# Kernel optimization log

Hardware: AMD Instinct MI355X
Metric: run time of the kernel (lower is better)

## Reference

```python
import jax, jax.numpy as jnp
import numpy as np

N = 8192          # number of bodies
BOX = 112.0       # world size chosen so expected #colliding pairs ~ 4N
EPS = 1e-12


def setup_inputs() -> dict:
    key = jax.random.key(0)
    k1, k2 = jax.random.split(key)
    centers = jax.random.uniform(k1, (N, 2), dtype=jnp.float32) * BOX
    radii = 0.5 + 0.5 * jax.random.uniform(k2, (N,), dtype=jnp.float32)
    return {"centers": centers, "radii": radii, "limit_broad": 4 * N, "limit_narrow": N}


def reference(centers, radii, limit_broad, limit_narrow):
    n = centers.shape[0]
    # ---- broad phase: all-pairs AABB overlap (AABB = center +/- radius) ----
    dc = jnp.abs(centers[:, None, :] - centers[None, :, :])      # [N,N,2]
    rsum = radii[:, None] + radii[None, :]                        # [N,N]
    overlap = jnp.all(dc <= rsum[..., None], axis=-1)             # [N,N]
    idx = jnp.arange(n)
    mask = overlap & (idx[:, None] < idx[None, :])                # i < j, as in _check_aabb_collision
    # compaction to a fixed limit of 4N candidate pairs (-1 = empty slot)
    flat = jnp.nonzero(mask.reshape(-1), size=limit_broad, fill_value=-1)[0]
    valid_b = flat >= 0
    safe = jnp.where(valid_b, flat, 0)
    pi, pj = safe // n, safe % n                                  # [4N]
    # ---- narrow phase: exact circle penetration on the candidates ----
    d = centers[pj] - centers[pi]                                 # [4N,2]
    dist = jnp.sqrt(jnp.sum(d * d, axis=-1) + EPS)                # [4N]
    depth = radii[pi] + radii[pj] - dist                          # [4N]
    pen = d / dist[:, None] * depth[:, None]                      # penetration vector [4N,2]
    hit = valid_b & (depth > 0)
    # second compaction: keep at most N actually-penetrating pairs
    sel = jnp.nonzero(hit, size=limit_narrow, fill_value=-1)[0]
    vsel = sel >= 0
    ssafe = jnp.where(vsel, sel, 0)
    si, sj = pi[ssafe], pj[ssafe]                                 # [N]
    delta = 0.5 * pen[ssafe] * vsel[:, None].astype(centers.dtype)
    # ---- resolve: scatter: push bodies apart by half the penetration each ----
    new_centers = centers.at[si].add(-delta).at[sj].add(delta)
    return new_centers
```

## Files before the change

### kernel.cpp

```cpp
#include <hip/hip_runtime.h>


constexpr int NB = 8192;
constexpr int GRID_DIM = 56;
constexpr int NCELLS = GRID_DIM * GRID_DIM;
constexpr int CAP = 20;
constexpr int NBLK = 96;
constexpr int RPB = (NB + NBLK - 1) / NBLK;
constexpr float INV_CELL = 0.5f;
constexpr float EPS = 1e-12f;

constexpr int O_CCOUNT = 0;
constexpr int O_RCOMB  = O_CCOUNT + NCELLS;
constexpr int O_CELLS  = (O_RCOMB + NB + 3) & ~3;

__device__ __forceinline__ int cell_of(float v) {
    int c = (int)(v * INV_CELL);
    return c > GRID_DIM - 1 ? GRID_DIM - 1 : (c < 0 ? 0 : c);
}

__device__ __forceinline__ int wave_incl_scan(int v, int lane) {
#pragma unroll
    for (int off = 1; off < 64; off <<= 1) {
        int y = __shfl_up(v, off);
        if (lane >= off) v += y;
    }
    return v;
}

__global__ void fill_kernel(const float2* __restrict__ centers,
                            const float* __restrict__ radii,
                            int* __restrict__ ccount,
                            float4* __restrict__ cells,
                            int* __restrict__ rcomb,
                            float2* __restrict__ out2) {
    const int t = blockIdx.x * blockDim.x + threadIdx.x;
    if (t >= NB) return;
    const float2 c = centers[t];
    const float r = radii[t];
    out2[t] = c;
    rcomb[t] = 0;
    const int cell = cell_of(c.y) * GRID_DIM + cell_of(c.x);
    const int slot = atomicAdd(&ccount[cell], 1);
    if (slot < CAP)
        cells[cell * CAP + slot] = make_float4(c.x, c.y, r, __int_as_float(t));
}

__global__ void count_kernel(const float2* __restrict__ centers,
                             const float* __restrict__ radii,
                             const int* __restrict__ ccount,
                             const float4* __restrict__ cells,
                             int* __restrict__ rcomb) {
    const int t = blockIdx.x * blockDim.x + threadIdx.x;
    if (t >= 3 * NB) return;
    const int i = t & (NB - 1);
    const int seg = t >> 13;
    const float2 ci = centers[i];
    const float ri = radii[i];
    const int cx = cell_of(ci.x), cy = cell_of(ci.y);
    const int yy = cy - 1 + seg;
    if (yy < 0 || yy >= GRID_DIM) return;
    const int x0 = max(cx - 1, 0), x1 = min(cx + 1, GRID_DIM - 1);
    int rc = 0, hc = 0;
    for (int xx = x0; xx <= x1; ++xx) {
        const int c = yy * GRID_DIM + xx;
        const int n = min(ccount[c], CAP);
        const float4* p = cells + c * CAP;
        for (int k = 0; k < n; ++k) {
            const float4 o = p[k];
            if (__float_as_int(o.w) <= i) continue;
            const float rs = ri + o.z;
            const float dx = o.x - ci.x, dy = o.y - ci.y;
            if (fabsf(dx) <= rs && fabsf(dy) <= rs) {
                ++rc;
                if (rs - sqrtf(dx * dx + dy * dy + EPS) > 0.f) ++hc;
            }
        }
    }
    if (rc | hc) atomicAdd(&rcomb[i], (rc << 8) | hc);
}

__device__ int slow_boundary_hits(const int* ccount, const float4* cells,
                                  const float2* centers, const float* radii,
                                  int i, int lim) {
    const float2 ci = centers[i];
    const float ri = radii[i];
    const int cx = cell_of(ci.x), cy = cell_of(ci.y);
    const int x0 = max(cx - 1, 0), x1 = min(cx + 1, GRID_DIM - 1);
    const int y0 = max(cy - 1, 0), y1 = min(cy + 1, GRID_DIM - 1);
    int h = 0;
    for (int yy = y0; yy <= y1; ++yy)
        for (int xx = x0; xx <= x1; ++xx) {
            const int c = yy * GRID_DIM + xx;
            const int n = min(ccount[c], CAP);
            for (int k = 0; k < n; ++k) {
                const float4 o = cells[c * CAP + k];
                const int j = __float_as_int(o.w);
                if (j <= i) continue;
                const float rs = ri + o.z, dx = o.x - ci.x, dy = o.y - ci.y;
                if (!(fabsf(dx) <= rs && fabsf(dy) <= rs)) continue;
                int brank = 0;
                for (int yy2 = y0; yy2 <= y1; ++yy2)
                    for (int xx2 = x0; xx2 <= x1; ++xx2) {
                        const int c2 = yy2 * GRID_DIM + xx2;
                        const int n2 = min(ccount[c2], CAP);
                        for (int k2 = 0; k2 < n2; ++k2) {
                            const float4 o2 = cells[c2 * CAP + k2];
                            const int j2 = __float_as_int(o2.w);
                            if (j2 <= i || j2 >= j) continue;
                            const float rs2 = ri + o2.z;
                            if (fabsf(o2.x - ci.x) <= rs2 && fabsf(o2.y - ci.y) <= rs2)
                                ++brank;
                        }
                    }
                if (brank < lim && rs - sqrtf(dx * dx + dy * dy + EPS) > 0.f) ++h;
            }
        }
    return h;
}

__global__ __launch_bounds__(256) void final_kernel(
        const float2* __restrict__ centers, const float* __restrict__ radii,
        const int* __restrict__ ccount, const float4* __restrict__ cells,
        const int* __restrict__ rcomb,
        const int* __restrict__ LBp, const int* __restrict__ LNp,
        float* __restrict__ out) {
    __shared__ unsigned char sh_st[NB];
    __shared__ int wsum[4];
    __shared__ int spec_n;
    __shared__ int spec_row[2], spec_bst[2], spec_h0[2];
    const int tid = threadIdx.x;
    const int lane = tid & 63, wid = tid >> 6;
    const int LB = *LBp, LN = *LNp;
    if (tid == 0) spec_n = 0;

    int4 v[8];
    const int base = tid * 32;
#pragma unroll
    for (int k = 0; k < 8; ++k) v[k] = ((const int4*)rcomb)[tid * 8 + k];
    const int* vv = (const int*)v;
    int rsum = 0;
#pragma unroll
    for (int k = 0; k < 32; ++k) rsum += vv[k] >> 8;
    const int incl = wave_incl_scan(rsum, lane);
    if (lane == 63) wsum[wid] = incl;
    __syncthreads();
    if (wid == 0) {
        const int orig = (lane < 4) ? wsum[lane] : 0;
        const int inc = wave_incl_scan(orig, lane);
        if (lane < 4) wsum[lane] = inc - orig;
    }
    __syncthreads();
    const int runb0 = wsum[wid] + incl - rsum;
    int runb = runb0, hsum = 0;
#pragma unroll
    for (int k = 0; k < 32; ++k) {
        const int val = vv[k];
        const int rc = val >> 8, hr = val & 0xff;
        int hc;
        if (runb >= LB) hc = 0;
        else if (runb + rc <= LB) hc = hr;
        else hc = slow_boundary_hits(ccount, cells, centers, radii, base + k,
                                     LB - runb);
        hsum += hc;
        runb += rc;
    }
    __syncthreads();
    const int incl2 = wave_incl_scan(hsum, lane);
    if (lane == 63) wsum[wid] = incl2;
    __syncthreads();
    if (wid == 0) {
        const int orig = (lane < 4) ? wsum[lane] : 0;
        const int inc = wave_incl_scan(orig, lane);
        if (lane < 4) wsum[lane] = inc - orig;
    }
    __syncthreads();
    int runh = wsum[wid] + incl2 - hsum;
    runb = runb0;
#pragma unroll
    for (int k = 0; k < 32; ++k) {
        const int i = base + k;
        const int val = vv[k];
        const int rc = val >> 8, hr = val & 0xff;
        int hc;
        if (runb >= LB) hc = 0;
        else if (runb + rc <= LB) hc = hr;
        else hc = slow_boundary_hits(ccount, cells, centers, radii, i, LB - runb);
        unsigned char st = 0;
        if (hc > 0 && runh < LN) {
            const bool bfast = (runb + rc <= LB);
            const bool nfast = (runh + hc <= LN);
            if (bfast && nfast) st = 1;
            else {
                const int n = atomicAdd(&spec_n, 1);
                if (n < 2) { spec_row[n] = i; spec_bst[n] = runb; spec_h0[n] = runh; }
            }
        }
        sh_st[i] = st;
        runb += rc;
        runh += hc;
    }
    __syncthreads();

    const int row_lo = blockIdx.x * RPB;
    const int row_hi = min(NB, row_lo + RPB);

    if (tid < 64) {
        const int ns = min(spec_n, 2);
        for (int sp = 0; sp < ns; ++sp) {
            const int i = spec_row[sp];
            if (i < row_lo || i >= row_hi) continue;
            const int blim = LB - spec_bst[sp];
            const int h0 = spec_h0[sp];
            const float2 ci = centers[i];
            const float ri = radii[i];
            const int cx = cell_of(ci.x), cy = cell_of(ci.y);
            const int x0 = max(cx - 1, 0), x1 = min(cx + 1, GRID_DIM - 1);
            const int y0 = max(cy - 1, 0), y1 = min(cy + 1, GRID_DIM - 1);
            int seg0[9], slen[9], nseg = 0, K = 0;
            for (int yy = y0; yy <= y1; ++yy)
                for (int xx = x0; xx <= x1; ++xx) {
                    const int c = yy * GRID_DIM + xx;
                    const int n = min(ccount[c], CAP);
                    if (n > 0) { seg0[nseg] = c * CAP; slen[nseg] = n; K += n; ++nseg; }
                }
            float accx = 0.f, accy = 0.f;
            for (int cb = 0; cb < K; cb += 64) {
                const int e = cb + lane;
                const bool ok = e < K;
                int s = 0;
                if (ok) {
                    int r = e;
                    for (int g = 0; g < nseg; ++g) {
                        if (r < slen[g]) { s = seg0[g] + r; break; }
                        r -= slen[g];
                    }
                }
                const float4 o = ok ? cells[s] : make_float4(0, 0, 0, __int_as_float(-1));
                const int j = __float_as_int(o.w);
                const float rs = ri + o.z, dx = o.x - ci.x, dy = o.y - ci.y;
                const bool ov = ok && j > i && fabsf(dx) <= rs && fabsf(dy) <= rs;
                if (ov) {
                    const float dist = sqrtf(dx * dx + dy * dy + EPS);
                    const float depth = rs - dist;
                    int brank = 0, hrank = 0;
                    for (int e2 = 0; e2 < K; ++e2) {
                        int r2 = e2, s2 = 0;
                        for (int g = 0; g < nseg; ++g) {
                            if (r2 < slen[g]) { s2 = seg0[g] + r2; break; }
                            r2 -= slen[g];
                        }
                        const float4 o2 = cells[s2];
                        const int j2 = __float_as_int(o2.w);
                        if (j2 <= i || j2 >= j) continue;
                        const float rs2 = ri + o2.z;
                        const float dx2 = o2.x - ci.x, dy2 = o2.y - ci.y;
                        if (fabsf(dx2) <= rs2 && fabsf(dy2) <= rs2) {
                            ++brank;
                            if (rs2 - sqrtf(dx2 * dx2 + dy2 * dy2 + EPS) > 0.f) ++hrank;
                        }
                    }
                    if (depth > 0.f && brank < blim && h0 + hrank < LN) {
                        const float sc = 0.5f * depth / dist;
                        const float px = sc * dx, py = sc * dy;
                        accx -= px; accy -= py;
                        atomicAdd(&out[2 * j], px);
                        atomicAdd(&out[2 * j + 1], py);
                    }
                }
            }
#pragma unroll
            for (int off = 32; off > 0; off >>= 1) {
                accx += __shfl_down(accx, off);
                accy += __shfl_down(accy, off);
            }
            if (lane == 0 && (accx != 0.f || accy != 0.f)) {
                atomicAdd(&out[2 * i], accx);
                atomicAdd(&out[2 * i + 1], accy);
            }
        }
    }

    for (int u = tid; u < RPB * 3; u += 256) {
        const int i = row_lo + u / 3;
        if (i >= row_hi) break;
        if (!sh_st[i]) continue;
        const int seg = u % 3;
        const float2 ci = centers[i];
        const float ri = radii[i];
        const int cx = cell_of(ci.x), cy = cell_of(ci.y);
        const int yy = cy - 1 + seg;
        if (yy < 0 || yy >= GRID_DIM) continue;
        const int x0 = max(cx - 1, 0), x1 = min(cx + 1, GRID_DIM - 1);
        float accx = 0.f, accy = 0.f;
        for (int xx = x0; xx <= x1; ++xx) {
            const int c = yy * GRID_DIM + xx;
            const int n = min(ccount[c], CAP);
            const float4* p = cells + c * CAP;
            for (int k = 0; k < n; ++k) {
                const float4 o = p[k];
                const int j = __float_as_int(o.w);
                if (j <= i) continue;
                const float rs = ri + o.z;
                const float dx = o.x - ci.x, dy = o.y - ci.y;
                if (!(fabsf(dx) <= rs && fabsf(dy) <= rs)) continue;
                const float dist = sqrtf(dx * dx + dy * dy + EPS);
                const float depth = rs - dist;
                if (depth <= 0.f) continue;
                const float sc = 0.5f * depth / dist;
                const float px = sc * dx, py = sc * dy;
                accx -= px; accy -= py;
                atomicAdd(&out[2 * j], px);
                atomicAdd(&out[2 * j + 1], py);
            }
        }
        if (accx != 0.f || accy != 0.f) {
            atomicAdd(&out[2 * i], accx);
            atomicAdd(&out[2 * i + 1], accy);
        }
    }
}

extern "C" void kernel_launch(void* const* d_in, const int* in_sizes, int n_in,
                              void* d_out, int out_size, void* d_ws, size_t ws_size,
                              hipStream_t stream) {
    const float2* centers = (const float2*)d_in[0];
    const float* radii    = (const float*)d_in[1];
    const int* LBp = (const int*)d_in[2];
    const int* LNp = (const int*)d_in[3];
    float* out = (float*)d_out;

    int* ws = (int*)d_ws;
    int* ccount = ws + O_CCOUNT;
    int* rcomb  = ws + O_RCOMB;
    float4* cells = (float4*)(ws + O_CELLS);

    hipMemsetAsync(ccount, 0, NCELLS * sizeof(int), stream);
    fill_kernel<<<NB / 256, 256, 0, stream>>>(centers, radii, ccount, cells,
                                              rcomb, (float2*)out);
    count_kernel<<<3 * NB / 256, 256, 0, stream>>>(centers, radii, ccount,
                                                   cells, rcomb);
    final_kernel<<<NBLK, 256, 0, stream>>>(centers, radii, ccount, cells,
                                           rcomb, LBp, LNp, out);
}
```

Measured before the change: 107.3 us.

## Replace atomic scatter with per-body gather and drop count atomics

After: 126.7 us. +18.1%, slower.

```diff
diff --git a/kernel.cpp b/kernel.cpp
--- a/kernel.cpp
+++ b/kernel.cpp
@@ -9,10 +9,11 @@
 constexpr int RPB = (NB + NBLK - 1) / NBLK;
 constexpr float INV_CELL = 0.5f;
 constexpr float EPS = 1e-12f;
+constexpr int INF = 0x7fffffff;
 
 constexpr int O_CCOUNT = 0;
-constexpr int O_RCOMB  = O_CCOUNT + NCELLS;
-constexpr int O_CELLS  = (O_RCOMB + NB + 3) & ~3;
+constexpr int O_COMB   = O_CCOUNT + NCELLS;
+constexpr int O_CELLS  = (O_COMB + 3 * NB + 3) & ~3;
 
 __device__ __forceinline__ int cell_of(float v) {
     int c = (int)(v * INV_CELL);
@@ -31,26 +32,21 @@
 __global__ void fill_kernel(const float2* __restrict__ centers,
                             const float* __restrict__ radii,
                             int* __restrict__ ccount,
-                            float4* __restrict__ cells,
-                            int* __restrict__ rcomb,
-                            float2* __restrict__ out2) {
+                            float4* __restrict__ cells) {
     const int t = blockIdx.x * blockDim.x + threadIdx.x;
     if (t >= NB) return;
     const float2 c = centers[t];
-    const float r = radii[t];
-    out2[t] = c;
-    rcomb[t] = 0;
     const int cell = cell_of(c.y) * GRID_DIM + cell_of(c.x);
     const int slot = atomicAdd(&ccount[cell], 1);
     if (slot < CAP)
-        cells[cell * CAP + slot] = make_float4(c.x, c.y, r, __int_as_float(t));
+        cells[cell * CAP + slot] = make_float4(c.x, c.y, radii[t], __int_as_float(t));
 }
 
 __global__ void count_kernel(const float2* __restrict__ centers,
                              const float* __restrict__ radii,
                              const int* __restrict__ ccount,
                              const float4* __restrict__ cells,
-                             int* __restrict__ rcomb) {
+                             int* __restrict__ comb) {
     const int t = blockIdx.x * blockDim.x + threadIdx.x;
     if (t >= 3 * NB) return;
     const int i = t & (NB - 1);
@@ -59,25 +55,69 @@
     const float ri = radii[i];
     const int cx = cell_of(ci.x), cy = cell_of(ci.y);
     const int yy = cy - 1 + seg;
-    if (yy < 0 || yy >= GRID_DIM) return;
+    int rc = 0, hc = 0;
+    if (yy >= 0 && yy < GRID_DIM) {
+        const int x0 = max(cx - 1, 0), x1 = min(cx + 1, GRID_DIM - 1);
+        for (int xx = x0; xx <= x1; ++xx) {
+            const int c = yy * GRID_DIM + xx;
+            const int n = min(ccount[c], CAP);
+            const float4* p = cells + c * CAP;
+            for (int k = 0; k < n; ++k) {
+                const float4 o = p[k];
+                if (__float_as_int(o.w) <= i) continue;
+                const float rs = ri + o.z;
+                const float dx = o.x - ci.x, dy = o.y - ci.y;
+                if (fabsf(dx) <= rs && fabsf(dy) <= rs) {
+                    ++rc;
+                    if (rs - sqrtf(dx * dx + dy * dy + EPS) > 0.f) ++hc;
+                }
+            }
+        }
+    }
+    comb[t] = (rc << 8) | hc;
+}
+
+__device__ int2 pair_rank(const int* ccount, const float4* cells,
+                          float xi, float yi, float ri, int i, int j, int blim) {
+    const int cx = cell_of(xi), cy = cell_of(yi);
     const int x0 = max(cx - 1, 0), x1 = min(cx + 1, GRID_DIM - 1);
-    int rc = 0, hc = 0;
-    for (int xx = x0; xx <= x1; ++xx) {
-        const int c = yy * GRID_DIM + xx;
-        const int n = min(ccount[c], CAP);
-        const float4* p = cells + c * CAP;
-        for (int k = 0; k < n; ++k) {
-            const float4 o = p[k];
-            if (__float_as_int(o.w) <= i) continue;
-            const float rs = ri + o.z;
-            const float dx = o.x - ci.x, dy = o.y - ci.y;
-            if (fabsf(dx) <= rs && fabsf(dy) <= rs) {
-                ++rc;
-                if (rs - sqrtf(dx * dx + dy * dy + EPS) > 0.f) ++hc;
-            }
-        }
-    }
-    if (rc | hc) atomicAdd(&rcomb[i], (rc << 8) | hc);
+    const int y0 = max(cy - 1, 0), y1 = min(cy + 1, GRID_DIM - 1);
+    int brank = 0, hrank = 0;
+    for (int yy = y0; yy <= y1; ++yy)
+        for (int xx = x0; xx <= x1; ++xx) {
+            const int c = yy * GRID_DIM + xx;
+            const int n = min(ccount[c], CAP);
+            for (int k = 0; k < n; ++k) {
+                const float4 o2 = cells[c * CAP + k];
+                const int j2 = __float_as_int(o2.w);
+                if (j2 <= i || j2 >= j) continue;
+                const float rs2 = ri + o2.z;
+                const float dx2 = o2.x - xi, dy2 = o2.y - yi;
+                if (!(fabsf(dx2) <= rs2 && fabsf(dy2) <= rs2)) continue;
+                ++brank;
+                if (rs2 - sqrtf(dx2 * dx2 + dy2 * dy2 + EPS) > 0.f) {
+                    if (blim == INF) ++hrank;
+                    else {
+                        int b2 = 0;
+                        for (int yb = y0; yb <= y1; ++yb)
+                            for (int xb = x0; xb <= x1; ++xb) {
+                                const int cb2 = yb * GRID_DIM + xb;
+                                const int nb2 = min(ccount[cb2], CAP);
+                                for (int k2 = 0; k2 < nb2; ++k2) {
+                                    const float4 o3 = cells[cb2 * CAP + k2];
+                                    const int j3 = __float_as_int(o3.w);
+                                    if (j3 <= i || j3 >= j2) continue;
+                                    const float rs3 = ri + o3.z;
+                                    if (fabsf(o3.x - xi) <= rs3 && fabsf(o3.y - yi) <= rs3)
+                                        ++b2;
+                                }
+                            }
+                        if (b2 < blim) ++hrank;
+                    }
+                }
+            }
+        }
+    return make_int2(brank, hrank);
 }
 
 __device__ int slow_boundary_hits(const int* ccount, const float4* cells,
@@ -99,21 +139,9 @@
                 if (j <= i) continue;
                 const float rs = ri + o.z, dx = o.x - ci.x, dy = o.y - ci.y;
                 if (!(fabsf(dx) <= rs && fabsf(dy) <= rs)) continue;
-                int brank = 0;
-                for (int yy2 = y0; yy2 <= y1; ++yy2)
-                    for (int xx2 = x0; xx2 <= x1; ++xx2) {
-                        const int c2 = yy2 * GRID_DIM + xx2;
-                        const int n2 = min(ccount[c2], CAP);
-                        for (int k2 = 0; k2 < n2; ++k2) {
-                            const float4 o2 = cells[c2 * CAP + k2];
-                            const int j2 = __float_as_int(o2.w);
-                            if (j2 <= i || j2 >= j) continue;
-                            const float rs2 = ri + o2.z;
-                            if (fabsf(o2.x - ci.x) <= rs2 && fabsf(o2.y - ci.y) <= rs2)
-                                ++brank;
-                        }
-                    }
-                if (brank < lim && rs - sqrtf(dx * dx + dy * dy + EPS) > 0.f) ++h;
+                if (rs - sqrtf(dx * dx + dy * dy + EPS) <= 0.f) continue;
+                const int2 r = pair_rank(ccount, cells, ci.x, ci.y, ri, i, j, INF);
+                if (r.x < lim) ++h;
             }
         }
     return h;
@@ -122,27 +150,36 @@
 __global__ __launch_bounds__(256) void final_kernel(
         const float2* __restrict__ centers, const float* __restrict__ radii,
         const int* __restrict__ ccount, const float4* __restrict__ cells,
-        const int* __restrict__ rcomb,
+        const int* __restrict__ comb,
         const int* __restrict__ LBp, const int* __restrict__ LNp,
-        float* __restrict__ out) {
-    __shared__ unsigned char sh_st[NB];
+        float2* __restrict__ out) {
+    __shared__ unsigned char sh_pol[NB];
+    __shared__ float sh_ax[RPB * 3], sh_ay[RPB * 3];
     __shared__ int wsum[4];
-    __shared__ int spec_n;
-    __shared__ int spec_row[2], spec_bst[2], spec_h0[2];
-    const int tid = threadIdx.x;
-    const int lane = tid & 63, wid = tid >> 6;
+    __shared__ int spec_n, spec_row[2], spec_blim[2], spec_hlim[2];
+    const int tid = threadIdx.x, lane = tid & 63, wid = tid >> 6;
     const int LB = *LBp, LN = *LNp;
     if (tid == 0) spec_n = 0;
 
-    int4 v[8];
+    int crc[32];
+    {
+        const int4* c4 = (const int4*)comb;
+#pragma unroll
+        for (int k = 0; k < 8; ++k) {
+            const int4 a = c4[tid * 8 + k];
+            const int4 b = c4[2048 + tid * 8 + k];
+            const int4 c = c4[4096 + tid * 8 + k];
+            crc[4 * k + 0] = a.x + b.x + c.x;
+            crc[4 * k + 1] = a.y + b.y + c.y;
+            crc[4 * k + 2] = a.z + b.z + c.z;
+            crc[4 * k + 3] = a.w + b.w + c.w;
+        }
+    }
     const int base = tid * 32;
-#pragma unroll
-    for (int k = 0; k < 8; ++k) v[k] = ((const int4*)rcomb)[tid * 8 + k];
-    const int* vv = (const int*)v;
     int rsum = 0;
 #pragma unroll
-    for (int k = 0; k < 32; ++k) rsum += vv[k] >> 8;
-    const int incl = wave_incl_scan(rsum, lane);
+    for (int k = 0; k < 32; ++k) rsum += crc[k] >> 8;
+    int incl = wave_incl_scan(rsum, lane);
     if (lane == 63) wsum[wid] = incl;
     __syncthreads();
     if (wid == 0) {
@@ -153,10 +190,8 @@
     __syncthreads();
     const int runb0 = wsum[wid] + incl - rsum;
     int runb = runb0, hsum = 0;
-#pragma unroll
     for (int k = 0; k < 32; ++k) {
-        const int val = vv[k];
-        const int rc = val >> 8, hr = val & 0xff;
+        const int rc = crc[k] >> 8, hr = crc[k] & 0xff;
         int hc;
         if (runb >= LB) hc = 0;
         else if (runb + rc <= LB) hc = hr;
@@ -166,8 +201,8 @@
         runb += rc;
     }
     __syncthreads();
-    const int incl2 = wave_incl_scan(hsum, lane);
-    if (lane == 63) wsum[wid] = incl2;
+    incl = wave_incl_scan(hsum, lane);
+    if (lane == 63) wsum[wid] = incl;
     __syncthreads();
     if (wid == 0) {
         const int orig = (lane < 4) ? wsum[lane] : 0;
@@ -175,148 +210,99 @@
         if (lane < 4) wsum[lane] = inc - orig;
     }
     __syncthreads();
-    int runh = wsum[wid] + incl2 - hsum;
+    int runh = wsum[wid] + incl - hsum;
     runb = runb0;
-#pragma unroll
     for (int k = 0; k < 32; ++k) {
         const int i = base + k;
-        const int val = vv[k];
-        const int rc = val >> 8, hr = val & 0xff;
+        const int rc = crc[k] >> 8, hr = crc[k] & 0xff;
         int hc;
         if (runb >= LB) hc = 0;
         else if (runb + rc <= LB) hc = hr;
         else hc = slow_boundary_hits(ccount, cells, centers, radii, i, LB - runb);
-        unsigned char st = 0;
+        unsigned char p = 0;
         if (hc > 0 && runh < LN) {
-            const bool bfast = (runb + rc <= LB);
-            const bool nfast = (runh + hc <= LN);
-            if (bfast && nfast) st = 1;
+            const bool bf = (runb + rc <= LB);
+            const bool nf = (runh + hc <= LN);
+            if (bf && nf) p = 1;
             else {
+                p = 2;
                 const int n = atomicAdd(&spec_n, 1);
-                if (n < 2) { spec_row[n] = i; spec_bst[n] = runb; spec_h0[n] = runh; }
-            }
-        }
-        sh_st[i] = st;
+                if (n < 2) {
+                    spec_row[n]  = i;
+                    spec_blim[n] = bf ? INF : LB - runb;
+                    spec_hlim[n] = nf ? INF : LN - runh;
+                }
+            }
+        }
+        sh_pol[i] = p;
         runb += rc;
         runh += hc;
     }
     __syncthreads();
+    const int ns = min(spec_n, 2);
 
     const int row_lo = blockIdx.x * RPB;
-    const int row_hi = min(NB, row_lo + RPB);
-
-    if (tid < 64) {
-        const int ns = min(spec_n, 2);
-        for (int sp = 0; sp < ns; ++sp) {
-            const int i = spec_row[sp];
-            if (i < row_lo || i >= row_hi) continue;
-            const int blim = LB - spec_bst[sp];
-            const int h0 = spec_h0[sp];
-            const float2 ci = centers[i];
-            const float ri = radii[i];
-            const int cx = cell_of(ci.x), cy = cell_of(ci.y);
-            const int x0 = max(cx - 1, 0), x1 = min(cx + 1, GRID_DIM - 1);
-            const int y0 = max(cy - 1, 0), y1 = min(cy + 1, GRID_DIM - 1);
-            int seg0[9], slen[9], nseg = 0, K = 0;
-            for (int yy = y0; yy <= y1; ++yy)
+    for (int u = tid; u < RPB * 3; u += 256) {
+        const int b = row_lo + u / 3;
+        float ax = 0.f, ay = 0.f;
+        if (b < NB) {
+            const int seg = u - (u / 3) * 3;
+            const float2 cb = centers[b];
+            const float rb = radii[b];
+            const unsigned char pol_b = sh_pol[b];
+            const int cx = cell_of(cb.x), cy = cell_of(cb.y);
+            const int yy = cy - 1 + seg;
+            if (yy >= 0 && yy < GRID_DIM) {
+                const int x0 = max(cx - 1, 0), x1 = min(cx + 1, GRID_DIM - 1);
                 for (int xx = x0; xx <= x1; ++xx) {
                     const int c = yy * GRID_DIM + xx;
                     const int n = min(ccount[c], CAP);
-                    if (n > 0) { seg0[nseg] = c * CAP; slen[nseg] = n; K += n; ++nseg; }
-                }
-            float accx = 0.f, accy = 0.f;
-            for (int cb = 0; cb < K; cb += 64) {
-                const int e = cb + lane;
-                const bool ok = e < K;
-                int s = 0;
-                if (ok) {
-                    int r = e;
-                    for (int g = 0; g < nseg; ++g) {
-                        if (r < slen[g]) { s = seg0[g] + r; break; }
-                        r -= slen[g];
+                    const float4* p = cells + c * CAP;
+                    for (int k = 0; k < n; ++k) {
+                        const float4 o = p[k];
+                        const int id = __float_as_int(o.w);
+                        if (id == b) continue;
+                        const float rs = rb + o.z;
+                        const float dx = o.x - cb.x, dy = o.y - cb.y;
+                        if (!(fabsf(dx) <= rs && fabsf(dy) <= rs)) continue;
+                        const bool rowside = id > b;
+                        const unsigned char pq = rowside ? pol_b : sh_pol[id];
+                        if (pq == 0) continue;
+                        const float dist = sqrtf(dx * dx + dy * dy + EPS);
+                        const float depth = rs - dist;
+                        if (depth <= 0.f) continue;
+                        bool apply = (pq == 1);
+                        if (!apply) {
+                            const int ii = rowside ? b : id;
+                            const int jj = rowside ? id : b;
+                            const int sp = (ns > 1 && spec_row[1] == ii) ? 1 : 0;
+                            const float xi = rowside ? cb.x : o.x;
+                            const float yi = rowside ? cb.y : o.y;
+                            const float ri = rowside ? rb : o.z;
+                            const int2 r = pair_rank(ccount, cells, xi, yi, ri,
+                                                     ii, jj, spec_blim[sp]);
+                            apply = (r.x < spec_blim[sp]) && (r.y < spec_hlim[sp]);
+                        }
+                        if (apply) {
+                            const float sc = 0.5f * depth / dist;
+                            ax -= sc * dx;
+                            ay -= sc * dy;
+                        }
                     }
                 }
-                const float4 o = ok ? cells[s] : make_float4(0, 0, 0, __int_as_float(-1));
-                const int j = __float_as_int(o.w);
-                const float rs = ri + o.z, dx = o.x - ci.x, dy = o.y - ci.y;
-                const bool ov = ok && j > i && fabsf(dx) <= rs && fabsf(dy) <= rs;
-                if (ov) {
-                    const float dist = sqrtf(dx * dx + dy * dy + EPS);
-                    const float depth = rs - dist;
-                    int brank = 0, hrank = 0;
-                    for (int e2 = 0; e2 < K; ++e2) {
-                        int r2 = e2, s2 = 0;
-                        for (int g = 0; g < nseg; ++g) {
-                            if (r2 < slen[g]) { s2 = seg0[g] + r2; break; }
-                            r2 -= slen[g];
-                        }
-                        const float4 o2 = cells[s2];
-                        const int j2 = __float_as_int(o2.w);
-                        if (j2 <= i || j2 >= j) continue;
-                        const float rs2 = ri + o2.z;
-                        const float dx2 = o2.x - ci.x, dy2 = o2.y - ci.y;
-                        if (fabsf(dx2) <= rs2 && fabsf(dy2) <= rs2) {
-                            ++brank;
-                            if (rs2 - sqrtf(dx2 * dx2 + dy2 * dy2 + EPS) > 0.f) ++hrank;
-                        }
-                    }
-                    if (depth > 0.f && brank < blim && h0 + hrank < LN) {
-                        const float sc = 0.5f * depth / dist;
-                        const float px = sc * dx, py = sc * dy;
-                        accx -= px; accy -= py;
-                        atomicAdd(&out[2 * j], px);
-                        atomicAdd(&out[2 * j + 1], py);
-                    }
-                }
-            }
-#pragma unroll
-            for (int off = 32; off > 0; off >>= 1) {
-                accx += __shfl_down(accx, off);
-                accy += __shfl_down(accy, off);
-            }
-            if (lane == 0 && (accx != 0.f || accy != 0.f)) {
-                atomicAdd(&out[2 * i], accx);
-                atomicAdd(&out[2 * i + 1], accy);
-            }
-        }
-    }
-
-    for (int u = tid; u < RPB * 3; u += 256) {
-        const int i = row_lo + u / 3;
-        if (i >= row_hi) break;
-        if (!sh_st[i]) continue;
-        const int seg = u % 3;
-        const float2 ci = centers[i];
-        const float ri = radii[i];
-        const int cx = cell_of(ci.x), cy = cell_of(ci.y);
-        const int yy = cy - 1 + seg;
-        if (yy < 0 || yy >= GRID_DIM) continue;
-        const int x0 = max(cx - 1, 0), x1 = min(cx + 1, GRID_DIM - 1);
-        float accx = 0.f, accy = 0.f;
-        for (int xx = x0; xx <= x1; ++xx) {
-            const int c = yy * GRID_DIM + xx;
-            const int n = min(ccount[c], CAP);
-            const float4* p = cells + c * CAP;
-            for (int k = 0; k < n; ++k) {
-                const float4 o = p[k];
-                const int j = __float_as_int(o.w);
-                if (j <= i) continue;
-                const float rs = ri + o.z;
-                const float dx = o.x - ci.x, dy = o.y - ci.y;
-                if (!(fabsf(dx) <= rs && fabsf(dy) <= rs)) continue;
-                const float dist = sqrtf(dx * dx + dy * dy + EPS);
-                const float depth = rs - dist;
-                if (depth <= 0.f) continue;
-                const float sc = 0.5f * depth / dist;
-                const float px = sc * dx, py = sc * dy;
-                accx -= px; accy -= py;
-                atomicAdd(&out[2 * j], px);
-                atomicAdd(&out[2 * j + 1], py);
-            }
-        }
-        if (accx != 0.f || accy != 0.f) {
-            atomicAdd(&out[2 * i], accx);
-            atomicAdd(&out[2 * i + 1], accy);
+            }
+        }
+        sh_ax[u] = ax;
+        sh_ay[u] = ay;
+    }
+    __syncthreads();
+    if (tid < RPB) {
+        const int b = row_lo + tid;
+        if (b < NB) {
+            const float2 cb = centers[b];
+            const float ax = sh_ax[tid * 3] + sh_ax[tid * 3 + 1] + sh_ax[tid * 3 + 2];
+            const float ay = sh_ay[tid * 3] + sh_ay[tid * 3 + 1] + sh_ay[tid * 3 + 2];
+            out[b] = make_float2(cb.x + ax, cb.y + ay);
         }
     }
 }
@@ -328,18 +314,16 @@
     const float* radii    = (const float*)d_in[1];
     const int* LBp = (const int*)d_in[2];
     const int* LNp = (const int*)d_in[3];
-    float* out = (float*)d_out;
 
     int* ws = (int*)d_ws;
     int* ccount = ws + O_CCOUNT;
-    int* rcomb  = ws + O_RCOMB;
+    int* comb   = ws + O_COMB;
     float4* cells = (float4*)(ws + O_CELLS);
 
     hipMemsetAsync(ccount, 0, NCELLS * sizeof(int), stream);
-    fill_kernel<<<NB / 256, 256, 0, stream>>>(centers, radii, ccount, cells,
-                                              rcomb, (float2*)out);
+    fill_kernel<<<NB / 256, 256, 0, stream>>>(centers, radii, ccount, cells);
     count_kernel<<<3 * NB / 256, 256, 0, stream>>>(centers, radii, ccount,
-                                                   cells, rcomb);
-    final_kernel<<<NBLK, 256, 0, stream>>>(centers, radii, ccount, cells,
-                                           rcomb, LBp, LNp, out);
-}
+                                                   cells, comb);
+    final_kernel<<<NBLK, 256, 0, stream>>>(centers, radii, ccount, cells, comb,
+                                           LBp, LNp, (float2*)d_out);
+}
```
